# Performance work log

Measured on AMD Instinct MI355X. Metric: run time of the kernel, lower is better.

Reference implementation:

```python
import jax, jax.numpy as jnp
import numpy as np

# FP4 E2M1 constants (from the torch module)
EXP_BITS = 2
EXP_BIAS = 1          # 2**(EXP_BITS-1) - 1
MANT_BITS = 1
MAX_EXP_FIELD = 3     # (1 << EXP_BITS) - 1
MIN_NORMAL_EXP = 0    # 1 - EXP_BIAS
FP4_MAX = 6.0         # (1 + 1/2) * 2**(MAX_EXP_FIELD-1 - EXP_BIAS + 1) = 1.5 * 4
GROUP = 128


def fp4_quant_dequant(x):
    """Faithful composition of _float_to_fp4 followed by _fp4_to_float (E2M1,
    subnormal-aware), expressed in float arithmetic (bit pack/unpack cancels)."""
    a = jnp.abs(x)
    zero_mask = a == 0
    a_safe = jnp.where(zero_mask, jnp.float32(1e-8), a)
    e = jnp.floor(jnp.log2(a_safe))                      # unbiased exponent
    is_sub = e < MIN_NORMAL_EXP
    e_c = jnp.clip(e, MIN_NORMAL_EXP, MAX_EXP_FIELD - EXP_BIAS)
    mant_scale = float(1 << MANT_BITS)                   # 2.0
    mant_normal = jnp.clip(jnp.round((a_safe / jnp.exp2(e_c) - 1.0) * mant_scale), 0.0, mant_scale - 1.0)
    mant_sub = jnp.clip(jnp.round(a_safe / (2.0 ** MIN_NORMAL_EXP) * mant_scale), 0.0, mant_scale - 1.0)
    mant = jnp.where(is_sub, mant_sub, mant_normal)
    # decode (_fp4_to_float): normals (1 + m/2)*2^(e), subnormals (m/2)*2^(1-bias)
    val_normal = (1.0 + mant / mant_scale) * jnp.exp2(e_c)
    val_sub = (mant / mant_scale) * (2.0 ** (1 - EXP_BIAS))
    val = jnp.where(is_sub, val_sub, val_normal)
    val = jnp.where(x < 0, -val, val)
    return jnp.where(zero_mask, jnp.zeros_like(val), val)


def setup_inputs() -> dict:
    key = jax.random.key(0)
    k1, k2, k3 = jax.random.split(key, 3)
    x = jax.random.normal(k1, (4096, 4096), dtype=jnp.float32)
    weight = jax.random.normal(k2, (4096, 4096), dtype=jnp.float32) * 0.02
    b = jax.random.normal(k3, (4096,), dtype=jnp.float32)
    return {"x": x, "weight": weight, "b": b}


def reference(x, weight, b):
    out_f, in_f = weight.shape
    wg = weight.reshape(out_f, in_f // GROUP, GROUP)
    amax = jnp.max(jnp.abs(wg), axis=-1, keepdims=True)       # [out, groups, 1]
    scale = jnp.where(amax == 0, jnp.float32(1.0), amax / FP4_MAX)
    w_deq = (fp4_quant_dequant(wg / scale) * scale).reshape(out_f, in_f)
    return x @ w_deq.T + b
```

## Files before the change

kernel.cpp:

```cpp
#include <hip/hip_runtime.h>
#include <hip/hip_bf16.h>
#include <stdint.h>

#define KDIM 4096
#define NDIM 4096
#define MDIM 4096
#define BM 256
#define BN 256
#define BK 64

typedef __attribute__((ext_vector_type(8))) short bf16x8;
typedef __attribute__((ext_vector_type(4))) float f32x4;


__device__ __forceinline__ unsigned short bf16bits(float f) {
    union { float f; uint32_t u; } c; c.f = f;
    uint32_t u = c.u;
    uint32_t r = (u + 0x7fffu + ((u >> 16) & 1u)) >> 16;
    return (unsigned short)r;
}

__device__ __forceinline__ float fp4qd(float x) {
    float a = fabsf(x);
    if (a == 0.0f) return 0.0f;
    float e = floorf(log2f(a));
    float val;
    if (e < 0.0f) {
        float mant = fminf(fmaxf(rintf(a * 2.0f), 0.0f), 1.0f);
        val = mant * 0.5f;
    } else {
        float ec = fminf(e, 2.0f);
        float p  = exp2f(ec);
        float mant = fminf(fmaxf(rintf((a / p - 1.0f) * 2.0f), 0.0f), 1.0f);
        val = (1.0f + 0.5f * mant) * p;
    }
    return (x < 0.0f) ? -val : val;
}

__device__ __forceinline__ void gld16(void* lds, const void* g) {
    __builtin_amdgcn_global_load_lds(
        (const __attribute__((address_space(1))) unsigned int*)g,
        (__attribute__((address_space(3))) unsigned int*)lds,
        16, 0, 0);
}

__global__ __launch_bounds__(256) void wdeq_kernel(const float* __restrict__ W,
                                                   unsigned short* __restrict__ Wq) {
    int grp = blockIdx.x * 4 + (threadIdx.x >> 6);
    int l = threadIdx.x & 63;
    const float* gp = W + (size_t)grp * 128 + l * 2;
    float2 v = *(const float2*)gp;
    float am = fmaxf(fabsf(v.x), fabsf(v.y));
    #pragma unroll
    for (int s = 32; s; s >>= 1) am = fmaxf(am, __shfl_xor(am, s));
    float scale = (am == 0.0f) ? 1.0f : am / 6.0f;
    float q0 = fp4qd(v.x / scale) * scale;
    float q1 = fp4qd(v.y / scale) * scale;
    ushort2 o;
    o.x = bf16bits(q0);
    o.y = bf16bits(q1);
    *(ushort2*)(Wq + (size_t)grp * 128 + l * 2) = o;
}

__global__ __launch_bounds__(256) void xcvt_kernel(const float* __restrict__ X,
                                                   unsigned short* __restrict__ Xb) {
    size_t i = (size_t)(blockIdx.x * 256 + threadIdx.x) * 4;
    float4 v = *(const float4*)(X + i);
    ushort4 o;
    o.x = bf16bits(v.x); o.y = bf16bits(v.y);
    o.z = bf16bits(v.z); o.w = bf16bits(v.w);
    *(ushort4*)(Xb + i) = o;
}


#define BAR()    __builtin_amdgcn_s_barrier()
#define LGKM0()  asm volatile("s_waitcnt lgkmcnt(0)" ::: "memory")
#define LGKM8()  asm volatile("s_waitcnt lgkmcnt(8)" ::: "memory")
#define VM6()    asm volatile("s_waitcnt vmcnt(6)" ::: "memory")
#define SCH0()   __builtin_amdgcn_sched_barrier(0)
#define PRIO(x)  __builtin_amdgcn_s_setprio(x)

__global__ __launch_bounds__(512, 2) void gemm256(const unsigned short* __restrict__ A,
                                                  const unsigned short* __restrict__ B,
                                                  const float* __restrict__ bias,
                                                  float* __restrict__ C) {
    __shared__ __attribute__((aligned(16))) char smem[2][2][4][8192];
    char* sm = (char*)&smem[0][0][0][0];

    const int t = threadIdx.x;
    const int l = t & 63;
    const int w = __builtin_amdgcn_readfirstlane(t >> 6);
    const int wm = w >> 2;
    const int wn = w & 3;

    int bid = blockIdx.x;
    int swz = (bid & 7) * 32 + (bid >> 3);
    int brow = (swz >> 4) * BM;
    int bcol = (swz & 15) * BN;

    const int lr8  = l >> 3;
    const int slot = l & 7;
    const int scol = (slot ^ lr8) << 3;
    const unsigned short* pA = A + (size_t)(brow + w * 8 + lr8) * KDIM + scol;
    const unsigned short* pB = B + (size_t)(bcol + w * 8 + lr8) * KDIM + scol;

#define STAGE64(b, op, slab, kt) do {                                          \
    const unsigned short* _s = ((op) ? pB : pA)                                \
        + (size_t)((slab) * 64) * KDIM + (size_t)(kt) * BK;                    \
    gld16(sm + (b) * 65536 + (op) * 32768 + (slab) * 8192 + w * 1024, _s);     \
} while (0)

    const int fr  = l & 15;
    const int fq  = l >> 4;
    const int kx0 = ((fq    ) ^ (fr & 7)) << 4;
    const int kx1 = ((fq + 4) ^ (fr & 7)) << 4;
    const int frA = fr * 128;

#define RD_A(b, mh) do {                                                        \
    const char* _p = sm + (b) * 65536 + wm * 16384 + (mh) * 8192 + frA;         \
    _Pragma("unroll")                                                           \
    for (int m = 0; m < 4; ++m) {                                               \
        a[m][0] = *(const bf16x8*)(_p + m * 2048 + kx0);                        \
        a[m][1] = *(const bf16x8*)(_p + m * 2048 + kx1);                        \
    }                                                                           \
} while (0)

#define RD_B(b, nh, arr) do {                                                   \
    const char* _p = sm + (b) * 65536 + 32768 + wn * 8192 + (nh) * 4096 + frA;  \
    _Pragma("unroll")                                                           \
    for (int n = 0; n < 2; ++n) {                                               \
        arr[n][0] = *(const bf16x8*)(_p + n * 2048 + kx0);                      \
        arr[n][1] = *(const bf16x8*)(_p + n * 2048 + kx1);                      \
    }                                                                           \
} while (0)

#define MM(mh, nh, arr)                                                         \
    _Pragma("unroll")                                                           \
    for (int m = 0; m < 4; ++m)                                                 \
        _Pragma("unroll")                                                       \
        for (int n = 0; n < 2; ++n)                                             \
            _Pragma("unroll")                                                   \
            for (int ks = 0; ks < 2; ++ks)                                      \
                acc[(mh) * 4 + m][(nh) * 2 + n] =                               \
                    __builtin_amdgcn_mfma_f32_16x16x32_bf16(                    \
                        a[m][ks], arr[n][ks], acc[(mh) * 4 + m][(nh) * 2 + n],  \
                        0, 0, 0);

    f32x4 acc[8][4];
    #pragma unroll
    for (int m = 0; m < 8; ++m)
        #pragma unroll
        for (int n = 0; n < 4; ++n)
            acc[m][n] = f32x4{0.f, 0.f, 0.f, 0.f};

    bf16x8 a[4][2], bA[2][2], bB[2][2];

    STAGE64(0, 0, 0, 0); STAGE64(0, 0, 2, 0); STAGE64(0, 1, 0, 0); STAGE64(0, 1, 1, 0);
    STAGE64(0, 1, 2, 0); STAGE64(0, 1, 3, 0); STAGE64(0, 0, 1, 0); STAGE64(0, 0, 3, 0);
    STAGE64(1, 0, 0, 1); STAGE64(1, 0, 2, 1); STAGE64(1, 1, 0, 1); STAGE64(1, 1, 1, 1);
    STAGE64(1, 1, 2, 1); STAGE64(1, 1, 3, 1);
    VM6();
    BAR();

    for (int it = 0; it < 32; ++it) {
        const int k1 = 2 * it + 1;
        const int k2 = (2 * it + 2) & 63;
        const int k3 = (2 * it + 3) & 63;

        RD_A(0, 0); RD_B(0, 0, bA);
        STAGE64(1, 0, 1, k1); STAGE64(1, 0, 3, k1);
        LGKM8();
        BAR(); LGKM0(); SCH0();
        PRIO(1); MM(0, 0, bA); PRIO(0);
        BAR();
        RD_B(0, 1, bB);
        STAGE64(0, 0, 0, k2); STAGE64(0, 0, 2, k2);
        BAR(); LGKM0(); SCH0();
        PRIO(1); MM(0, 1, bB); PRIO(0);
        BAR();
        RD_A(0, 1);
        STAGE64(0, 1, 0, k2); STAGE64(0, 1, 1, k2);
        BAR(); LGKM0(); SCH0();
        PRIO(1); MM(1, 1, bB); PRIO(0);
        BAR();
        STAGE64(0, 1, 2, k2); STAGE64(0, 1, 3, k2);
        BAR(); SCH0();
        PRIO(1); MM(1, 0, bA); PRIO(0);
        VM6();
        BAR();
        RD_A(1, 0); RD_B(1, 0, bA);
        STAGE64(0, 0, 1, k2); STAGE64(0, 0, 3, k2);
        LGKM8();
        BAR(); LGKM0(); SCH0();
        PRIO(1); MM(0, 0, bA); PRIO(0);
        BAR();
        RD_B(1, 1, bB);
        STAGE64(1, 0, 0, k3); STAGE64(1, 0, 2, k3);
        BAR(); LGKM0(); SCH0();
        PRIO(1); MM(0, 1, bB); PRIO(0);
        BAR();
        RD_A(1, 1);
        STAGE64(1, 1, 0, k3); STAGE64(1, 1, 1, k3);
        BAR(); LGKM0(); SCH0();
        PRIO(1); MM(1, 1, bB); PRIO(0);
        BAR();
        STAGE64(1, 1, 2, k3); STAGE64(1, 1, 3, k3);
        BAR(); SCH0();
        PRIO(1); MM(1, 0, bA); PRIO(0);
        VM6();
        BAR();
    }

    float bb[4];
    #pragma unroll
    for (int n = 0; n < 4; ++n) bb[n] = bias[bcol + wn * 64 + n * 16 + fr];
    #pragma unroll
    for (int mi = 0; mi < 8; ++mi) {
        #pragma unroll
        for (int q = 0; q < 4; ++q) {
            int row = brow + wm * 128 + mi * 16 + fq * 4 + q;
            float* crow = C + (size_t)row * NDIM + bcol + wn * 64;
            #pragma unroll
            for (int n = 0; n < 4; ++n)
                crow[n * 16 + fr] = acc[mi][n][q] + bb[n];
        }
    }
}

extern "C" void kernel_launch(void* const* d_in, const int* in_sizes, int n_in,
                              void* d_out, int out_size, void* d_ws, size_t ws_size,
                              hipStream_t stream) {
    const float* x = (const float*)d_in[0];
    const float* w = (const float*)d_in[1];
    const float* b = (const float*)d_in[2];
    float* out = (float*)d_out;

    unsigned short* xb = (unsigned short*)d_ws;
    unsigned short* wq = xb + (size_t)NDIM * KDIM;

    xcvt_kernel<<<MDIM * KDIM / 4 / 256, 256, 0, stream>>>(x, xb);
    wdeq_kernel<<<NDIM * (KDIM / 128) / 4, 256, 0, stream>>>(w, wq);
    gemm256<<<(MDIM / BM) * (NDIM / BN), 512, 0, stream>>>(xb, wq, b, out);
}
```

Measured before the change: 157.5 us.

## Double-buffer register fragments and prefetch LDS reads ahead of MFMA phases

Splits the A and B register fragments into even/odd sets so LDS reads for the next MFMA quarter are issued before the current quarter's MFMAs run. It also reorders the global-to-LDS staging schedule and replaces full lgkmcnt(0) and vmcnt(6) waits with partial waits. The goal is to hide LDS read latency behind matrix math. The cost is more fragment registers, which adds occupancy pressure at 2 waves per SIMD, and the hand-tuned waitcnt values risk reading LDS before it is ready.

```diff
diff --git a/kernel.cpp b/kernel.cpp
--- a/kernel.cpp
+++ b/kernel.cpp
@@ -74,9 +74,8 @@
 
 
 #define BAR()    __builtin_amdgcn_s_barrier()
-#define LGKM0()  asm volatile("s_waitcnt lgkmcnt(0)" ::: "memory")
-#define LGKM8()  asm volatile("s_waitcnt lgkmcnt(8)" ::: "memory")
-#define VM6()    asm volatile("s_waitcnt vmcnt(6)" ::: "memory")
+#define LGKM(n)  asm volatile("s_waitcnt lgkmcnt(" #n ")" ::: "memory")
+#define VM(n)    asm volatile("s_waitcnt vmcnt(" #n ")" ::: "memory")
 #define SCH0()   __builtin_amdgcn_sched_barrier(0)
 #define PRIO(x)  __builtin_amdgcn_s_setprio(x)
 
@@ -116,12 +115,12 @@
     const int kx1 = ((fq + 4) ^ (fr & 7)) << 4;
     const int frA = fr * 128;
 
-#define RD_A(b, mh) do {                                                        \
+#define RD_A(b, mh, arr) do {                                                   \
     const char* _p = sm + (b) * 65536 + wm * 16384 + (mh) * 8192 + frA;         \
     _Pragma("unroll")                                                           \
     for (int m = 0; m < 4; ++m) {                                               \
-        a[m][0] = *(const bf16x8*)(_p + m * 2048 + kx0);                        \
-        a[m][1] = *(const bf16x8*)(_p + m * 2048 + kx1);                        \
+        arr[m][0] = *(const bf16x8*)(_p + m * 2048 + kx0);                      \
+        arr[m][1] = *(const bf16x8*)(_p + m * 2048 + kx1);                      \
     }                                                                           \
 } while (0)
 
@@ -134,16 +133,16 @@
     }                                                                           \
 } while (0)
 
-#define MM(mh, nh, arr)                                                         \
+#define MM(mh, nh, A_, B_)                                                      \
     _Pragma("unroll")                                                           \
-    for (int m = 0; m < 4; ++m)                                                 \
+    for (int ks = 0; ks < 2; ++ks)                                              \
         _Pragma("unroll")                                                       \
-        for (int n = 0; n < 2; ++n)                                             \
+        for (int m = 0; m < 4; ++m)                                             \
             _Pragma("unroll")                                                   \
-            for (int ks = 0; ks < 2; ++ks)                                      \
+            for (int n = 0; n < 2; ++n)                                         \
                 acc[(mh) * 4 + m][(nh) * 2 + n] =                               \
                     __builtin_amdgcn_mfma_f32_16x16x32_bf16(                    \
-                        a[m][ks], arr[n][ks], acc[(mh) * 4 + m][(nh) * 2 + n],  \
+                        A_[m][ks], B_[n][ks], acc[(mh) * 4 + m][(nh) * 2 + n],  \
                         0, 0, 0);
 
     f32x4 acc[8][4];
@@ -153,61 +152,71 @@
         for (int n = 0; n < 4; ++n)
             acc[m][n] = f32x4{0.f, 0.f, 0.f, 0.f};
 
-    bf16x8 a[4][2], bA[2][2], bB[2][2];
+    bf16x8 aE[4][2], aO[4][2], bE[2][2], bO[2][2];
 
     STAGE64(0, 0, 0, 0); STAGE64(0, 0, 2, 0); STAGE64(0, 1, 0, 0); STAGE64(0, 1, 1, 0);
-    STAGE64(0, 1, 2, 0); STAGE64(0, 1, 3, 0); STAGE64(0, 0, 1, 0); STAGE64(0, 0, 3, 0);
+    STAGE64(0, 0, 1, 0); STAGE64(0, 0, 3, 0); STAGE64(0, 1, 2, 0); STAGE64(0, 1, 3, 0);
     STAGE64(1, 0, 0, 1); STAGE64(1, 0, 2, 1); STAGE64(1, 1, 0, 1); STAGE64(1, 1, 1, 1);
-    STAGE64(1, 1, 2, 1); STAGE64(1, 1, 3, 1);
-    VM6();
+    STAGE64(1, 0, 1, 1); STAGE64(1, 0, 3, 1); STAGE64(1, 1, 2, 1); STAGE64(1, 1, 3, 1);
+    VM(0);
     BAR();
+    RD_A(0, 0, aE);
+    RD_B(0, 0, bE);
 
     for (int it = 0; it < 32; ++it) {
-        const int k1 = 2 * it + 1;
         const int k2 = (2 * it + 2) & 63;
         const int k3 = (2 * it + 3) & 63;
 
-        RD_A(0, 0); RD_B(0, 0, bA);
-        STAGE64(1, 0, 1, k1); STAGE64(1, 0, 3, k1);
-        LGKM8();
-        BAR(); LGKM0(); SCH0();
-        PRIO(1); MM(0, 0, bA); PRIO(0);
-        BAR();
-        RD_B(0, 1, bB);
+        SCH0();
+        RD_B(0, 1, bO);
+        BAR(); LGKM(4); SCH0();
+        PRIO(1); MM(0, 0, aE, bE); PRIO(0);
+        BAR();
+        SCH0();
+        RD_A(0, 1, aO);
         STAGE64(0, 0, 0, k2); STAGE64(0, 0, 2, k2);
-        BAR(); LGKM0(); SCH0();
-        PRIO(1); MM(0, 1, bB); PRIO(0);
-        BAR();
-        RD_A(0, 1);
+        BAR(); LGKM(8); SCH0();
+        PRIO(1); MM(0, 1, aE, bO); PRIO(0);
+        VM(8);
+        BAR();
+        SCH0();
+        RD_A(1, 0, aE);
         STAGE64(0, 1, 0, k2); STAGE64(0, 1, 1, k2);
-        BAR(); LGKM0(); SCH0();
-        PRIO(1); MM(1, 1, bB); PRIO(0);
-        BAR();
+        BAR(); LGKM(8); SCH0();
+        PRIO(1); MM(1, 1, aO, bO); PRIO(0);
+        VM(4);
+        BAR();
+        SCH0();
+        STAGE64(0, 0, 1, k2); STAGE64(0, 0, 3, k2);
         STAGE64(0, 1, 2, k2); STAGE64(0, 1, 3, k2);
         BAR(); SCH0();
-        PRIO(1); MM(1, 0, bA); PRIO(0);
-        VM6();
-        BAR();
-        RD_A(1, 0); RD_B(1, 0, bA);
-        STAGE64(0, 0, 1, k2); STAGE64(0, 0, 3, k2);
-        LGKM8();
-        BAR(); LGKM0(); SCH0();
-        PRIO(1); MM(0, 0, bA); PRIO(0);
-        BAR();
-        RD_B(1, 1, bB);
+        PRIO(1); MM(1, 0, aO, bE); PRIO(0);
+        RD_B(1, 0, bE);
+        BAR();
+        SCH0();
+        RD_B(1, 1, bO);
+        BAR(); LGKM(4); SCH0();
+        PRIO(1); MM(0, 0, aE, bE); PRIO(0);
+        BAR();
+        SCH0();
+        RD_A(1, 1, aO);
         STAGE64(1, 0, 0, k3); STAGE64(1, 0, 2, k3);
-        BAR(); LGKM0(); SCH0();
-        PRIO(1); MM(0, 1, bB); PRIO(0);
-        BAR();
-        RD_A(1, 1);
+        BAR(); LGKM(8); SCH0();
+        PRIO(1); MM(0, 1, aE, bO); PRIO(0);
+        VM(2);
+        BAR();
+        SCH0();
+        RD_A(0, 0, aE);
         STAGE64(1, 1, 0, k3); STAGE64(1, 1, 1, k3);
-        BAR(); LGKM0(); SCH0();
-        PRIO(1); MM(1, 1, bB); PRIO(0);
-        BAR();
+        BAR(); LGKM(8); SCH0();
+        PRIO(1); MM(1, 1, aO, bO); PRIO(0);
+        BAR();
+        SCH0();
+        STAGE64(1, 0, 1, k3); STAGE64(1, 0, 3, k3);
         STAGE64(1, 1, 2, k3); STAGE64(1, 1, 3, k3);
         BAR(); SCH0();
-        PRIO(1); MM(1, 0, bA); PRIO(0);
-        VM6();
+        PRIO(1); MM(1, 0, aO, bE); PRIO(0);
+        RD_B(0, 0, bE);
         BAR();
     }
 
```

New measurement: 160.8 us. 2.1% more time.
